# Performance work log

Measured on AMD Instinct MI355X. Metric: run time of the kernel, lower is better.

Reference implementation:

```python
import jax, jax.numpy as jnp
import numpy as np

B, S, H, NH, BLK, R = 2, 4096, 768, 12, 64, 3
D = H // NH
NB = S // BLK
PENALTY = -10000.0


def setup_inputs() -> dict:
    key = jax.random.key(0)
    ks = jax.random.split(key, 5)
    return {
        "hidden_states": jax.random.normal(ks[0], (B, S, H), dtype=jnp.float32),
        "Wq": jax.random.normal(ks[1], (H, H), dtype=jnp.float32) * 0.02,
        "Wk": jax.random.normal(ks[2], (H, H), dtype=jnp.float32) * 0.02,
        "Wv": jax.random.normal(ks[3], (H, H), dtype=jnp.float32) * 0.02,
        "band_mask": jnp.ones((B, 1, NB - 4, BLK, 3 * BLK), dtype=jnp.float32),
        "from_mask": jnp.ones((B, 1, S, 1), dtype=jnp.float32),
        "to_mask": jnp.ones((B, 1, 1, S), dtype=jnp.float32),
        "from_blocked_mask": jnp.ones((B, NB, BLK), dtype=jnp.float32),
        "to_blocked_mask": jnp.ones((B, NB, BLK), dtype=jnp.float32),
        "rand_attn": jax.random.randint(ks[4], (B, NH, NB - 2, R), 0, NB, dtype=jnp.int64),
    }


def reference(hidden_states, Wq, Wk, Wv, band_mask, from_mask, to_mask,
              from_blocked_mask, to_blocked_mask, rand_attn):
    b, s, _ = hidden_states.shape
    nb, blk, r = NB, BLK, R
    rsqrt_d = 1.0 / jnp.sqrt(jnp.float32(D))
    sm = jax.nn.softmax

    # projections -> [b, h, s, d]
    def proj(W):
        return jnp.einsum('bse,ed->bsd', hidden_states, W).reshape(b, s, NH, D).transpose(0, 2, 1, 3)
    q, k, v = proj(Wq), proj(Wk), proj(Wv)

    bq = q.reshape(b, NH, nb, blk, D)
    bk = k.reshape(b, NH, nb, blk, D)
    bv = v.reshape(b, NH, nb, blk, D)

    # gather random key/value blocks: [b, h, nb-2, r*blk, d]
    bi = jnp.arange(b)[:, None, None, None]
    hi = jnp.arange(NH)[None, :, None, None]
    gk = bk[bi, hi, rand_attn].reshape(b, NH, nb - 2, r * blk, D)
    gv = bv[bi, hi, rand_attn].reshape(b, NH, nb - 2, r * blk, D)

    # random mask: [b, h, nb-2, blk, r*blk]
    rm = to_blocked_mask[jnp.arange(b)[:, None, None, None], rand_attn]  # [b,h,nb-2,r,blk]
    rm = rm.reshape(b, NH, nb - 2, r * blk)
    rand_mask = jnp.einsum('blq,bhlk->bhlqk', from_blocked_mask[:, 1:-1], rm)

    ones_rand = jnp.ones((b, 1, 1, r * blk), dtype=to_mask.dtype)
    ones_4blk = jnp.ones((b, NH, blk, 4 * blk), dtype=rand_mask.dtype)

    # --- first (global) block: attends to everything ---
    fp = jnp.einsum('bhqd,bhkd->bhqk', bq[:, :, 0], k) * rsqrt_d + (1.0 - to_mask) * PENALTY
    fc = jnp.einsum('bhqk,bhkd->bhqd', sm(fp, axis=-1), v)[:, :, None]  # [b,h,1,blk,d]

    # --- second block: first 3 blocks + last block + random blocks ---
    sk = jnp.concatenate([bk[:, :, 0], bk[:, :, 1], bk[:, :, 2], bk[:, :, -1], gk[:, :, 0]], axis=2)
    sv = jnp.concatenate([bv[:, :, 0], bv[:, :, 1], bv[:, :, 2], bv[:, :, -1], gv[:, :, 0]], axis=2)
    sp = jnp.einsum('bhqd,bhkd->bhqk', bq[:, :, 1], sk) * rsqrt_d
    seq_pad = jnp.concatenate([to_mask[:, :, :, :3 * blk], to_mask[:, :, :, -blk:], ones_rand], axis=3)
    rand_pad = jnp.concatenate([ones_4blk, rand_mask[:, :, 0]], axis=3)
    sp = sp + (1.0 - jnp.minimum(seq_pad, rand_pad)) * PENALTY
    sc = jnp.einsum('bhqk,bhkd->bhqd', sm(sp, axis=-1), sv)[:, :, None]

    # --- middle blocks: sliding window + global first/last + random ---
    ek = jnp.concatenate([bk[:, :, 1:-3], bk[:, :, 2:-2], bk[:, :, 3:-1]], axis=3)  # [b,h,nb-4,3blk,d]
    ev = jnp.concatenate([bv[:, :, 1:-3], bv[:, :, 2:-2], bv[:, :, 3:-1]], axis=3)
    mq = bq[:, :, 2:-2]
    inner = jnp.einsum('bhlqd,bhlkd->bhlqk', mq, ek) * rsqrt_d + (1.0 - band_mask) * PENALTY
    randb = jnp.einsum('bhlqd,bhlkd->bhlqk', mq, gk[:, :, 1:-1]) * rsqrt_d + (1.0 - rand_mask[:, :, 1:-1]) * PENALTY
    firstb = jnp.einsum('bhlqd,bhkd->bhlqk', mq, bk[:, :, 0]) * rsqrt_d + (1.0 - to_mask[:, :, :, None, :blk]) * PENALTY
    lastb = jnp.einsum('bhlqd,bhkd->bhlqk', mq, bk[:, :, -1]) * rsqrt_d + (1.0 - to_mask[:, :, :, None, -blk:]) * PENALTY
    band = jnp.concatenate([firstb, inner, randb, lastb], axis=-1)  # [...,(5+r)*blk]
    aw = sm(band, axis=-1)
    ctx_mid = (jnp.einsum('bhlqk,bhlkd->bhlqd', aw[..., blk:4 * blk], ev)
               + jnp.einsum('bhlqk,bhlkd->bhlqd', aw[..., 4 * blk:-blk], gv[:, :, 1:-1])
               + jnp.einsum('bhlqk,bhkd->bhlqd', aw[..., :blk], bv[:, :, 0])
               + jnp.einsum('bhlqk,bhkd->bhlqd', aw[..., -blk:], bv[:, :, -1]))

    # --- second-last block ---
    slk = jnp.concatenate([bk[:, :, 0], bk[:, :, -3], bk[:, :, -2], bk[:, :, -1], gk[:, :, -1]], axis=2)
    slv = jnp.concatenate([bv[:, :, 0], bv[:, :, -3], bv[:, :, -2], bv[:, :, -1], gv[:, :, -1]], axis=2)
    slp = jnp.einsum('bhqd,bhkd->bhqk', bq[:, :, -2], slk) * rsqrt_d
    sl_seq_pad = jnp.concatenate([to_mask[:, :, :, :blk], to_mask[:, :, :, -3 * blk:], ones_rand], axis=3)
    sl_rand_pad = jnp.concatenate([ones_4blk, rand_mask[:, :, -1]], axis=3)
    slp = slp + (1.0 - jnp.minimum(sl_seq_pad, sl_rand_pad)) * PENALTY
    slc = jnp.einsum('bhqk,bhkd->bhqd', sm(slp, axis=-1), slv)[:, :, None]

    # --- last (global) block ---
    lp = jnp.einsum('bhqd,bhkd->bhqk', bq[:, :, -1], k) * rsqrt_d + (1.0 - to_mask) * PENALTY
    lc = jnp.einsum('bhqk,bhkd->bhqd', sm(lp, axis=-1), v)[:, :, None]

    ctx = jnp.concatenate([fc, sc, ctx_mid, slc, lc], axis=2).reshape(b, NH, s, D)
    ctx = ctx * from_mask  # [b,1,s,1] broadcast
    return ctx.transpose(0, 2, 1, 3).reshape(b, s, NH * D)
```

## Files before the change

kernel.cpp:

```cpp
#include <hip/hip_runtime.h>
#include <hip/hip_bf16.h>
#include <stdint.h>

#define NHD 12
#define SLEN 4096
#define DH 64
#define NBLK 64
#define HDIM 768
#define PEN -10000.0f
#define LOG2E 1.44269504f

typedef __bf16 bf16x8 __attribute__((ext_vector_type(8)));
typedef float f32x4 __attribute__((ext_vector_type(4)));
typedef unsigned short u16x8 __attribute__((ext_vector_type(8)));

__device__ __forceinline__ unsigned short f2bf(float x) {
    union { float f; unsigned u; } v; v.f = x;
    unsigned r = v.u + 0x7fffu + ((v.u >> 16) & 1u);
    return (unsigned short)(r >> 16);
}

__device__ __forceinline__ void gl2lds16(const void* g, void* l) {
    __builtin_amdgcn_global_load_lds(
        (const __attribute__((address_space(1))) void*)g,
        (__attribute__((address_space(3))) void*)l, 16, 0, 0);
}

__global__ void k_cast_hs(const float* __restrict__ in, unsigned short* __restrict__ out, int n8) {
    int i = blockIdx.x * blockDim.x + threadIdx.x;
    if (i >= n8) return;
    const float4* p = (const float4*)in + (size_t)i * 2;
    float4 a = p[0], b = p[1];
    u16x8 o;
    o[0]=f2bf(a.x); o[1]=f2bf(a.y); o[2]=f2bf(a.z); o[3]=f2bf(a.w);
    o[4]=f2bf(b.x); o[5]=f2bf(b.y); o[6]=f2bf(b.z); o[7]=f2bf(b.w);
    ((u16x8*)out)[i] = o;
}

__global__ void k_wt(const float* __restrict__ Wq, const float* __restrict__ Wk,
                     const float* __restrict__ Wv, unsigned short* __restrict__ wt) {
    const float* W = blockIdx.z == 0 ? Wq : (blockIdx.z == 1 ? Wk : Wv);
    unsigned short* out = wt + (size_t)blockIdx.z * HDIM * HDIM;
    __shared__ float tile[64][65];
    int t = threadIdx.x;
    int k0 = blockIdx.x * 64, n0 = blockIdx.y * 64;
    int r = t >> 2, c4 = t & 3;
#pragma unroll
    for (int j = 0; j < 16; j += 4) {
        float4 v = *(const float4*)&W[(size_t)(k0 + r) * HDIM + n0 + c4 * 16 + j];
        tile[r][c4*16+j+0] = v.x; tile[r][c4*16+j+1] = v.y;
        tile[r][c4*16+j+2] = v.z; tile[r][c4*16+j+3] = v.w;
    }
    __syncthreads();
    u16x8 o0, o1;
#pragma unroll
    for (int j = 0; j < 8; ++j) o0[j] = f2bf(tile[c4*16 + j][r]);
#pragma unroll
    for (int j = 0; j < 8; ++j) o1[j] = f2bf(tile[c4*16 + 8 + j][r]);
    *(u16x8*)&out[(size_t)(n0 + r) * HDIM + k0 + c4*16]     = o0;
    *(u16x8*)&out[(size_t)(n0 + r) * HDIM + k0 + c4*16 + 8] = o1;
}

template<bool TR>
__global__ __launch_bounds__(256) void k_proj(const unsigned short* __restrict__ hsb,
                                              const unsigned short* __restrict__ wtb,
                                              unsigned short* __restrict__ outbuf) {
    __shared__ __align__(16) unsigned short As[8192];
    __shared__ __align__(16) unsigned short Bs[8192];
    const char* Abase = (const char*)hsb;
    const char* Bbase = (const char*)(wtb + (size_t)blockIdx.z * HDIM * HDIM);
    unsigned short* out = outbuf + (size_t)blockIdx.z * (2u * NHD * SLEN * DH);
    int m0 = blockIdx.x * 128, n0 = blockIdx.y * 128;
    int t = threadIdx.x;
    int w = t >> 6, l = t & 63, g = l >> 4, c = l & 15;
    int wm = w >> 1, wn = w & 1;
    int lr = l >> 3, ls = l & 7, sw = ls ^ lr;
    int c7 = c & 7;
    f32x4 acc[4][4];
#pragma unroll
    for (int i = 0; i < 4; ++i)
#pragma unroll
        for (int j = 0; j < 4; ++j) acc[i][j] = (f32x4){0.f,0.f,0.f,0.f};

    for (int kt = 0; kt < HDIM; kt += 64) {
        __syncthreads();
#pragma unroll
        for (int i = 0; i < 4; ++i) {
            int rowb = w * 32 + i * 8;
            gl2lds16(Abase + (size_t)(m0 + rowb + lr) * 1536 + kt * 2 + sw * 16,
                     (char*)As + rowb * 128);
            gl2lds16(Bbase + (size_t)(n0 + rowb + lr) * 1536 + kt * 2 + sw * 16,
                     (char*)Bs + rowb * 128);
        }
        __syncthreads();
#pragma unroll
        for (int ks = 0; ks < 2; ++ks) {
            bf16x8 af[4], bf_[4];
#pragma unroll
            for (int mt = 0; mt < 4; ++mt)
                af[mt]  = *(const bf16x8*)((const char*)As
                            + (64*wm + 16*mt + c) * 128 + (((ks*4 + g) ^ c7) * 16));
#pragma unroll
            for (int nt = 0; nt < 4; ++nt)
                bf_[nt] = *(const bf16x8*)((const char*)Bs
                            + (64*wn + 16*nt + c) * 128 + (((ks*4 + g) ^ c7) * 16));
#pragma unroll
            for (int i = 0; i < 4; ++i)
#pragma unroll
                for (int j = 0; j < 4; ++j)
                    acc[i][j] = TR
                        ? __builtin_amdgcn_mfma_f32_16x16x32_bf16(bf_[i], af[j], acc[i][j], 0, 0, 0)
                        : __builtin_amdgcn_mfma_f32_16x16x32_bf16(af[i], bf_[j], acc[i][j], 0, 0, 0);
        }
    }
#pragma unroll
    for (int i = 0; i < 4; ++i)
#pragma unroll
        for (int j = 0; j < 4; ++j)
#pragma unroll
            for (int r2 = 0; r2 < 4; ++r2) {
                if (!TR) {
                    int m = m0 + 64*wm + 16*i + 4*g + r2;
                    int n = n0 + 64*wn + 16*j + c;
                    int bb = m >> 12, s = m & 4095;
                    int hh = n >> 6,  d = n & 63;
                    out[(((size_t)bb * NHD + hh) * SLEN + s) * DH + d] = f2bf(acc[i][j][r2]);
                } else {
                    int n = n0 + 64*wn + 16*i + 4*g + r2;
                    int m = m0 + 64*wm + 16*j + c;
                    int bb = m >> 12, s = m & 4095;
                    int hh = n >> 6,  d = n & 63;
                    out[(((size_t)bb * NHD + hh) * DH + d) * SLEN + s] = f2bf(acc[i][j][r2]);
                }
            }
}

__global__ __launch_bounds__(256) void k_attn(
    const unsigned short* __restrict__ Qb, const unsigned short* __restrict__ Kb,
    const unsigned short* __restrict__ VTb,
    const int* __restrict__ rand_attn,
    const float* __restrict__ band_mask, const float* __restrict__ from_mask,
    const float* __restrict__ to_mask, const float* __restrict__ fbm,
    const float* __restrict__ tbm,
    float* __restrict__ out, float* __restrict__ partials)
{
    __shared__ __align__(16) unsigned short Kt[2][4096];
    __shared__ __align__(16) unsigned short Vt[2][4096];
    __shared__ __align__(16) char plds[4 * 2048];

    const float SC = 0.125f * LOG2E;
    const float PL = PEN * LOG2E;
    const float THR2 = 8.0f * LOG2E;

    int i0 = blockIdx.x;
    int gid = (i0 & 7) * 234 + (i0 >> 3);
    int bh = gid / 78, task = gid - bh * 78;
    int b = bh / NHD, h = bh - b * NHD;
    int t = threadIdx.x;
    int wq = t >> 6, l = t & 63, g = l >> 4, c = l & 15;
    int lr = l >> 3, ls = l & 7, sw = ls ^ lr;

    int row, mode = 0, pslot = 0;
    int blkj[8], kvj[8], sbj[8];
#pragma unroll
    for (int j = 0; j < 8; ++j) sbj[j] = 0;
    if (task < 8) {
        row = 0; mode = 1; pslot = task;
#pragma unroll
        for (int j = 0; j < 8; ++j) { blkj[j] = task * 8 + j; kvj[j] = 0; }
    } else if (task >= 70) {
        row = 63; mode = 1; pslot = task - 70;
#pragma unroll
        for (int j = 0; j < 8; ++j) { blkj[j] = pslot * 8 + j; kvj[j] = 0; }
    } else {
        row = task - 7;
        int rbase = ((b * NHD + h) * 62 + (row - 1)) * 3;
        blkj[4] = rand_attn[rbase];
        blkj[5] = rand_attn[rbase + 1];
        blkj[6] = rand_attn[rbase + 2];
        kvj[4] = kvj[5] = kvj[6] = 2;
        blkj[0] = 0; kvj[0] = 0;
        if (row == 1) {
            blkj[1]=1;  blkj[2]=2;  blkj[3]=63; kvj[1]=kvj[2]=kvj[3]=0;
            blkj[7]=0;  kvj[7]=3;
        } else if (row == 62) {
            blkj[1]=61; blkj[2]=62; blkj[3]=63; kvj[1]=kvj[2]=kvj[3]=0;
            blkj[7]=0;  kvj[7]=3;
        } else {
            blkj[1]=row-1; blkj[2]=row; blkj[3]=row+1;
            kvj[1]=kvj[2]=kvj[3]=1; sbj[1]=0; sbj[2]=64; sbj[3]=128;
            blkj[7]=63; kvj[7]=0;
        }
    }

    size_t bhoff = (size_t)bh * SLEN * DH;
    const char* Kbase = (const char*)(Kb + bhoff);
    const char* Vbase = (const char*)(VTb + (size_t)bh * DH * SLEN);
    int q0 = row * 64 + wq * 16;

    bf16x8 qf[2];
#pragma unroll
    for (int kk = 0; kk < 2; ++kk)
        qf[kk] = *(const bf16x8*)&Qb[bhoff + (size_t)(q0 + c) * DH + kk * 32 + 8 * g];

    float fmq = fbm[(b * NBLK + row) * 64 + wq * 16 + c];
    size_t bm_base = ((size_t)(b * 60 + row - 2) * 64 + (wq * 16 + c)) * 192;
    int tm_base = b * SLEN;

    float m_run = -1e30f, l_run = 0.f;
    f32x4 o_acc[4];
#pragma unroll
    for (int dt = 0; dt < 4; ++dt) o_acc[dt] = (f32x4){0.f,0.f,0.f,0.f};

    char* myl = plds + wq * 2048 + c * 128;
    int swz = (c & 7) << 4;

    auto stage = [&](int blk, int nb) __attribute__((always_inline)) {
#pragma unroll
        for (int ii = 0; ii < 2; ++ii) {
            int i = wq * 2 + ii;
            const char* ksrc = Kbase + (size_t)blk * 8192 + (size_t)(i*8 + lr) * 128 + sw * 16;
            gl2lds16(ksrc, (char*)&Kt[nb][0] + i * 1024);
            const char* vsrc = Vbase + (size_t)(i*8 + lr) * 8192 + (size_t)blk * 128 + sw * 16;
            gl2lds16(vsrc, (char*)&Vt[nb][0] + i * 1024);
        }
    };

    auto loadpen = [&](int kv, int blk, int sb, float4* pen) __attribute__((always_inline)) {
        if (kv == 0) {
#pragma unroll
            for (int mt = 0; mt < 4; ++mt) {
                float4 mk = *(const float4*)&to_mask[tm_base + blk * 64 + mt * 16 + 4 * g];
                pen[mt].x = (1.f - mk.x) * PL; pen[mt].y = (1.f - mk.y) * PL;
                pen[mt].z = (1.f - mk.z) * PL; pen[mt].w = (1.f - mk.w) * PL;
            }
        } else if (kv == 1) {
#pragma unroll
            for (int mt = 0; mt < 4; ++mt) {
                float4 mk = *(const float4*)&band_mask[bm_base + sb + mt * 16 + 4 * g];
                pen[mt].x = (1.f - mk.x) * PL; pen[mt].y = (1.f - mk.y) * PL;
                pen[mt].z = (1.f - mk.z) * PL; pen[mt].w = (1.f - mk.w) * PL;
            }
        } else if (kv == 2) {
#pragma unroll
            for (int mt = 0; mt < 4; ++mt) {
                float4 tb = *(const float4*)&tbm[(size_t)(b * NBLK + blk) * 64 + mt * 16 + 4 * g];
                pen[mt].x = (1.f - fmq * tb.x) * PL; pen[mt].y = (1.f - fmq * tb.y) * PL;
                pen[mt].z = (1.f - fmq * tb.z) * PL; pen[mt].w = (1.f - fmq * tb.w) * PL;
            }
        }
    };

    auto compute = [&](int kv, int nb, const float4* pen) __attribute__((always_inline)) {
        if (kv == 3) return;
        int c7 = c & 7;
        bf16x8 kf[4][2];
#pragma unroll
        for (int mt = 0; mt < 4; ++mt)
#pragma unroll
            for (int kk = 0; kk < 2; ++kk)
                kf[mt][kk] = *(const bf16x8*)((const char*)&Kt[nb][0]
                              + (mt*16 + c) * 128 + (((kk*4 + g) ^ c7) * 16));

        f32x4 sa[4];
#pragma unroll
        for (int mt = 0; mt < 4; ++mt) sa[mt] = (f32x4){0.f,0.f,0.f,0.f};
#pragma unroll
        for (int kk = 0; kk < 2; ++kk)
#pragma unroll
            for (int mt = 0; mt < 4; ++mt)
                sa[mt] = __builtin_amdgcn_mfma_f32_16x16x32_bf16(kf[mt][kk], qf[kk], sa[mt], 0, 0, 0);

#pragma unroll
        for (int mt = 0; mt < 4; ++mt) {
            sa[mt][0] = sa[mt][0] * SC + pen[mt].x;
            sa[mt][1] = sa[mt][1] * SC + pen[mt].y;
            sa[mt][2] = sa[mt][2] * SC + pen[mt].z;
            sa[mt][3] = sa[mt][3] * SC + pen[mt].w;
        }

        float pm = -1e30f;
#pragma unroll
        for (int mt = 0; mt < 4; ++mt)
#pragma unroll
            for (int r2 = 0; r2 < 4; ++r2) pm = fmaxf(pm, sa[mt][r2]);
        pm = fmaxf(pm, __shfl_xor(pm, 16));
        pm = fmaxf(pm, __shfl_xor(pm, 32));
        if (__ballot(pm > m_run + THR2)) {
            bool need = pm > m_run + THR2;
            float mnew = need ? pm : m_run;
            float scale = exp2f(m_run - mnew);
            m_run = mnew;
            l_run *= scale;
#pragma unroll
            for (int dt = 0; dt < 4; ++dt)
#pragma unroll
                for (int r2 = 0; r2 < 4; ++r2) o_acc[dt][r2] *= scale;
        }

        float rs = 0.f;
#pragma unroll
        for (int mt = 0; mt < 4; ++mt)
#pragma unroll
            for (int r2 = 0; r2 < 4; ++r2) {
                float e = exp2f(sa[mt][r2] - m_run);
                sa[mt][r2] = e;
                rs += e;
            }
        rs += __shfl_xor(rs, 16);
        rs += __shfl_xor(rs, 32);
        l_run += rs;

#pragma unroll
        for (int mt = 0; mt < 4; ++mt) {
            union { __bf16 hh[4]; unsigned long long u; } pk_;
            pk_.hh[0] = (__bf16)sa[mt][0]; pk_.hh[1] = (__bf16)sa[mt][1];
            pk_.hh[2] = (__bf16)sa[mt][2]; pk_.hh[3] = (__bf16)sa[mt][3];
            *(unsigned long long*)(myl + ((mt * 32 + g * 8) ^ swz)) = pk_.u;
        }
        asm volatile("" ::: "memory");
        bf16x8 pf0 = *(const bf16x8*)(myl + ((g * 16) ^ swz));
        bf16x8 pf1 = *(const bf16x8*)(myl + ((64 + g * 16) ^ swz));

#pragma unroll
        for (int dt = 0; dt < 4; ++dt) {
            bf16x8 v0 = *(const bf16x8*)((const char*)&Vt[nb][0]
                          + (dt*16 + c) * 128 + ((g ^ c7) * 16));
            bf16x8 v1 = *(const bf16x8*)((const char*)&Vt[nb][0]
                          + (dt*16 + c) * 128 + (((4 + g) ^ c7) * 16));
            o_acc[dt] = __builtin_amdgcn_mfma_f32_16x16x32_bf16(v0, pf0, o_acc[dt], 0, 0, 0);
            o_acc[dt] = __builtin_amdgcn_mfma_f32_16x16x32_bf16(v1, pf1, o_acc[dt], 0, 0, 0);
        }
    };

    float4 penA[4], penB[4];
    stage(blkj[0], 0);
    loadpen(kvj[0], blkj[0], sbj[0], penA);
    __syncthreads();
#pragma unroll
    for (int tt = 0; tt < 8; ++tt) {
        if (tt < 7) {
            stage(blkj[tt + 1], (tt & 1) ^ 1);
            loadpen(kvj[tt + 1], blkj[tt + 1], sbj[tt + 1], (tt & 1) ? penA : penB);
        }
        compute(kvj[tt], tt & 1, (tt & 1) ? penB : penA);
        __syncthreads();
    }

    if (mode == 0) {
        int s = q0 + c;
        float fm = from_mask[b * SLEN + s];
        float inv = fm / l_run;
        size_t obase = ((size_t)b * SLEN + s) * HDIM + h * DH;
#pragma unroll
        for (int dt = 0; dt < 4; ++dt) {
            float4 val;
            val.x = o_acc[dt][0] * inv;
            val.y = o_acc[dt][1] * inv;
            val.z = o_acc[dt][2] * inv;
            val.w = o_acc[dt][3] * inv;
            *(float4*)&out[obase + dt * 16 + 4 * g] = val;
        }
    } else {
        float* pb = partials + (size_t)((bh * 2 + (row == 63 ? 1 : 0)) * 8 + pslot) * 4224;
        int q = wq * 16 + c;
#pragma unroll
        for (int dt = 0; dt < 4; ++dt) {
            float4 val;
            val.x = o_acc[dt][0]; val.y = o_acc[dt][1];
            val.z = o_acc[dt][2]; val.w = o_acc[dt][3];
            *(float4*)&pb[q * 64 + dt * 16 + 4 * g] = val;
        }
        if (g == 0) {
            pb[4096 + q] = m_run;
            pb[4160 + q] = l_run;
        }
    }
}

__global__ void k_combine(const float* __restrict__ partials, const float* __restrict__ from_mask,
                          float* __restrict__ out) {
    int gid = blockIdx.x;
    int bh = gid >> 1, rb = gid & 1;
    int b = bh / NHD, h = bh - b * NHD;
    int t = threadIdx.x;
    int q = t >> 2, dc = (t & 3) * 16;
    const float* base = partials + (size_t)gid * 8 * 4224;
    float M = -1e30f;
#pragma unroll
    for (int i = 0; i < 8; ++i) M = fmaxf(M, base[i*4224 + 4096 + q]);
    float L = 0.f, cx[16];
#pragma unroll
    for (int j = 0; j < 16; ++j) cx[j] = 0.f;
    for (int i = 0; i < 8; ++i) {
        float w = exp2f(base[i*4224 + 4096 + q] - M);
        L += base[i*4224 + 4160 + q] * w;
#pragma unroll
        for (int j = 0; j < 16; ++j) cx[j] += base[i*4224 + q*64 + dc + j] * w;
    }
    int s = (rb ? 4032 : 0) + q;
    float fm = from_mask[b * SLEN + s];
    float inv = fm / L;
#pragma unroll
    for (int j = 0; j < 16; ++j)
        out[((size_t)b * SLEN + s) * HDIM + h * DH + dc + j] = cx[j] * inv;
}

extern "C" void kernel_launch(void* const* d_in, const int* in_sizes, int n_in,
                              void* d_out, int out_size, void* d_ws, size_t ws_size,
                              hipStream_t stream) {
    const float* hs    = (const float*)d_in[0];
    const float* Wq    = (const float*)d_in[1];
    const float* Wk    = (const float*)d_in[2];
    const float* Wv    = (const float*)d_in[3];
    const float* band  = (const float*)d_in[4];
    const float* fromm = (const float*)d_in[5];
    const float* tom   = (const float*)d_in[6];
    const float* fbm   = (const float*)d_in[7];
    const float* tbm   = (const float*)d_in[8];
    const int*   ra    = (const int*)d_in[9];
    float* out = (float*)d_out;

    char* ws = (char*)d_ws;
    unsigned short* hsb = (unsigned short*)(ws);
    unsigned short* wtb = (unsigned short*)(ws + 12582912);
    unsigned short* qkv = (unsigned short*)(ws + 16121856);
    float* partials     = (float*)(ws + 53870592);

    k_cast_hs<<<3072, 256, 0, stream>>>(hs, hsb, 786432);
    k_wt<<<dim3(12, 12, 3), 256, 0, stream>>>(Wq, Wk, Wv, wtb);
    k_proj<false><<<dim3(64, 6, 2), 256, 0, stream>>>(hsb, wtb, qkv);
    k_proj<true><<<dim3(64, 6, 1), 256, 0, stream>>>(hsb, wtb + 2 * HDIM * HDIM,
                                                     qkv + 2 * 6291456);
    k_attn<<<1872, 256, 0, stream>>>(qkv, qkv + 6291456, qkv + 2 * 6291456, ra,
                                     band, fromm, tom, fbm, tbm, out, partials);
    k_combine<<<48, 256, 0, stream>>>(partials, fromm, out);
}
```

Measured before the change: 109.7 us.

## Merge QKV projection launches and single-buffer V tile in attention kernel

The Q/K and transposed-V projection kernels are folded into one launch, with the weight selected from blockIdx.y and the transposed branch chosen at runtime. In the attention kernel, V is now single-buffered in LDS and is staged only after the PV step of the previous block, with an extra barrier per iteration. This cuts LDS use so more workgroups may fit per CU and removes one launch. In exchange it serializes the V load with compute and adds synchronization, and the projection kernel now carries a runtime branch around its MFMA loop.

After: 138.8 us. +26.6%, slower.

```diff
diff --git a/kernel.cpp b/kernel.cpp
--- a/kernel.cpp
+++ b/kernel.cpp
@@ -61,16 +61,16 @@
     *(u16x8*)&out[(size_t)(n0 + r) * HDIM + k0 + c4*16 + 8] = o1;
 }
 
-template<bool TR>
 __global__ __launch_bounds__(256) void k_proj(const unsigned short* __restrict__ hsb,
                                               const unsigned short* __restrict__ wtb,
-                                              unsigned short* __restrict__ outbuf) {
+                                              unsigned short* __restrict__ qkv) {
     __shared__ __align__(16) unsigned short As[8192];
     __shared__ __align__(16) unsigned short Bs[8192];
+    int z = blockIdx.y / 6, ny = blockIdx.y - z * 6;
     const char* Abase = (const char*)hsb;
-    const char* Bbase = (const char*)(wtb + (size_t)blockIdx.z * HDIM * HDIM);
-    unsigned short* out = outbuf + (size_t)blockIdx.z * (2u * NHD * SLEN * DH);
-    int m0 = blockIdx.x * 128, n0 = blockIdx.y * 128;
+    const char* Bbase = (const char*)(wtb + (size_t)z * HDIM * HDIM);
+    unsigned short* out = qkv + (size_t)z * (2u * NHD * SLEN * DH);
+    int m0 = blockIdx.x * 128, n0 = ny * 128;
     int t = threadIdx.x;
     int w = t >> 6, l = t & 63, g = l >> 4, c = l & 15;
     int wm = w >> 1, wn = w & 1;
@@ -104,13 +104,19 @@
             for (int nt = 0; nt < 4; ++nt)
                 bf_[nt] = *(const bf16x8*)((const char*)Bs
                             + (64*wn + 16*nt + c) * 128 + (((ks*4 + g) ^ c7) * 16));
-#pragma unroll
-            for (int i = 0; i < 4; ++i)
-#pragma unroll
-                for (int j = 0; j < 4; ++j)
-                    acc[i][j] = TR
-                        ? __builtin_amdgcn_mfma_f32_16x16x32_bf16(bf_[i], af[j], acc[i][j], 0, 0, 0)
-                        : __builtin_amdgcn_mfma_f32_16x16x32_bf16(af[i], bf_[j], acc[i][j], 0, 0, 0);
+            if (z != 2) {
+#pragma unroll
+                for (int i = 0; i < 4; ++i)
+#pragma unroll
+                    for (int j = 0; j < 4; ++j)
+                        acc[i][j] = __builtin_amdgcn_mfma_f32_16x16x32_bf16(af[i], bf_[j], acc[i][j], 0, 0, 0);
+            } else {
+#pragma unroll
+                for (int i = 0; i < 4; ++i)
+#pragma unroll
+                    for (int j = 0; j < 4; ++j)
+                        acc[i][j] = __builtin_amdgcn_mfma_f32_16x16x32_bf16(bf_[i], af[j], acc[i][j], 0, 0, 0);
+            }
         }
     }
 #pragma unroll
@@ -119,7 +125,7 @@
         for (int j = 0; j < 4; ++j)
 #pragma unroll
             for (int r2 = 0; r2 < 4; ++r2) {
-                if (!TR) {
+                if (z != 2) {
                     int m = m0 + 64*wm + 16*i + 4*g + r2;
                     int n = n0 + 64*wn + 16*j + c;
                     int bb = m >> 12, s = m & 4095;
@@ -145,7 +151,7 @@
     float* __restrict__ out, float* __restrict__ partials)
 {
     __shared__ __align__(16) unsigned short Kt[2][4096];
-    __shared__ __align__(16) unsigned short Vt[2][4096];
+    __shared__ __align__(16) unsigned short Vt[4096];
     __shared__ __align__(16) char plds[4 * 2048];
 
     const float SC = 0.125f * LOG2E;
@@ -215,14 +221,20 @@
     char* myl = plds + wq * 2048 + c * 128;
     int swz = (c & 7) << 4;
 
-    auto stage = [&](int blk, int nb) __attribute__((always_inline)) {
+    auto stageK = [&](int blk, int nb) __attribute__((always_inline)) {
 #pragma unroll
         for (int ii = 0; ii < 2; ++ii) {
             int i = wq * 2 + ii;
-            const char* ksrc = Kbase + (size_t)blk * 8192 + (size_t)(i*8 + lr) * 128 + sw * 16;
-            gl2lds16(ksrc, (char*)&Kt[nb][0] + i * 1024);
-            const char* vsrc = Vbase + (size_t)(i*8 + lr) * 8192 + (size_t)blk * 128 + sw * 16;
-            gl2lds16(vsrc, (char*)&Vt[nb][0] + i * 1024);
+            gl2lds16(Kbase + (size_t)blk * 8192 + (size_t)(i*8 + lr) * 128 + sw * 16,
+                     (char*)&Kt[nb][0] + i * 1024);
+        }
+    };
+    auto stageV = [&](int blk) __attribute__((always_inline)) {
+#pragma unroll
+        for (int ii = 0; ii < 2; ++ii) {
+            int i = wq * 2 + ii;
+            gl2lds16(Vbase + (size_t)(i*8 + lr) * 8192 + (size_t)blk * 128 + sw * 16,
+                     (char*)Vt + i * 1024);
         }
     };
 
@@ -251,8 +263,7 @@
         }
     };
 
-    auto compute = [&](int kv, int nb, const float4* pen) __attribute__((always_inline)) {
-        if (kv == 3) return;
+    auto qk_sm = [&](int nb, const float4* pen) __attribute__((always_inline)) {
         int c7 = c & 7;
         bf16x8 kf[4][2];
 #pragma unroll
@@ -261,7 +272,6 @@
             for (int kk = 0; kk < 2; ++kk)
                 kf[mt][kk] = *(const bf16x8*)((const char*)&Kt[nb][0]
                               + (mt*16 + c) * 128 + (((kk*4 + g) ^ c7) * 16));
-
         f32x4 sa[4];
 #pragma unroll
         for (int mt = 0; mt < 4; ++mt) sa[mt] = (f32x4){0.f,0.f,0.f,0.f};
@@ -270,7 +280,6 @@
 #pragma unroll
             for (int mt = 0; mt < 4; ++mt)
                 sa[mt] = __builtin_amdgcn_mfma_f32_16x16x32_bf16(kf[mt][kk], qf[kk], sa[mt], 0, 0, 0);
-
 #pragma unroll
         for (int mt = 0; mt < 4; ++mt) {
             sa[mt][0] = sa[mt][0] * SC + pen[mt].x;
@@ -278,7 +287,6 @@
             sa[mt][2] = sa[mt][2] * SC + pen[mt].z;
             sa[mt][3] = sa[mt][3] * SC + pen[mt].w;
         }
-
         float pm = -1e30f;
 #pragma unroll
         for (int mt = 0; mt < 4; ++mt)
@@ -297,7 +305,6 @@
 #pragma unroll
                 for (int r2 = 0; r2 < 4; ++r2) o_acc[dt][r2] *= scale;
         }
-
         float rs = 0.f;
 #pragma unroll
         for (int mt = 0; mt < 4; ++mt)
@@ -310,7 +317,6 @@
         rs += __shfl_xor(rs, 16);
         rs += __shfl_xor(rs, 32);
         l_run += rs;
-
 #pragma unroll
         for (int mt = 0; mt < 4; ++mt) {
             union { __bf16 hh[4]; unsigned long long u; } pk_;
@@ -319,14 +325,17 @@
             *(unsigned long long*)(myl + ((mt * 32 + g * 8) ^ swz)) = pk_.u;
         }
         asm volatile("" ::: "memory");
+    };
+
+    auto pv = [&]() __attribute__((always_inline)) {
+        int c7 = c & 7;
         bf16x8 pf0 = *(const bf16x8*)(myl + ((g * 16) ^ swz));
         bf16x8 pf1 = *(const bf16x8*)(myl + ((64 + g * 16) ^ swz));
-
 #pragma unroll
         for (int dt = 0; dt < 4; ++dt) {
-            bf16x8 v0 = *(const bf16x8*)((const char*)&Vt[nb][0]
+            bf16x8 v0 = *(const bf16x8*)((const char*)Vt
                           + (dt*16 + c) * 128 + ((g ^ c7) * 16));
-            bf16x8 v1 = *(const bf16x8*)((const char*)&Vt[nb][0]
+            bf16x8 v1 = *(const bf16x8*)((const char*)Vt
                           + (dt*16 + c) * 128 + (((4 + g) ^ c7) * 16));
             o_acc[dt] = __builtin_amdgcn_mfma_f32_16x16x32_bf16(v0, pf0, o_acc[dt], 0, 0, 0);
             o_acc[dt] = __builtin_amdgcn_mfma_f32_16x16x32_bf16(v1, pf1, o_acc[dt], 0, 0, 0);
@@ -334,17 +343,23 @@
     };
 
     float4 penA[4], penB[4];
-    stage(blkj[0], 0);
+    stageK(blkj[0], 0);
+    stageV(blkj[0]);
     loadpen(kvj[0], blkj[0], sbj[0], penA);
     __syncthreads();
 #pragma unroll
     for (int tt = 0; tt < 8; ++tt) {
+        int nb = tt & 1;
         if (tt < 7) {
-            stage(blkj[tt + 1], (tt & 1) ^ 1);
-            loadpen(kvj[tt + 1], blkj[tt + 1], sbj[tt + 1], (tt & 1) ? penA : penB);
-        }
-        compute(kvj[tt], tt & 1, (tt & 1) ? penB : penA);
+            stageK(blkj[tt + 1], nb ^ 1);
+            loadpen(kvj[tt + 1], blkj[tt + 1], sbj[tt + 1], nb ? penA : penB);
+        }
+        bool active = (kvj[tt] != 3);
+        if (active) qk_sm(nb, nb ? penB : penA);
         __syncthreads();
+        if (active) pv();
+        __syncthreads();
+        if (tt < 7) stageV(blkj[tt + 1]);
     }
 
     if (mode == 0) {
@@ -429,9 +444,7 @@
 
     k_cast_hs<<<3072, 256, 0, stream>>>(hs, hsb, 786432);
     k_wt<<<dim3(12, 12, 3), 256, 0, stream>>>(Wq, Wk, Wv, wtb);
-    k_proj<false><<<dim3(64, 6, 2), 256, 0, stream>>>(hsb, wtb, qkv);
-    k_proj<true><<<dim3(64, 6, 1), 256, 0, stream>>>(hsb, wtb + 2 * HDIM * HDIM,
-                                                     qkv + 2 * 6291456);
+    k_proj<<<dim3(64, 18), 256, 0, stream>>>(hsb, wtb, qkv);
     k_attn<<<1872, 256, 0, stream>>>(qkv, qkv + 6291456, qkv + 2 * 6291456, ra,
                                      band, fromm, tom, fbm, tbm, out, partials);
     k_combine<<<48, 256, 0, stream>>>(partials, fromm, out);
```

## Process two key blocks per attention step with 128-wide KV tiles

Applied to the files above, without the earlier changes.

The attention loop now stages two 64-key blocks at a time into doubled LDS buffers and runs one softmax/PV update over 128 keys. This halves the loop iterations, barriers and online-softmax rescale checks. V is staged in a new interleaved, swizzled layout so the PV MFMAs can use K=128. In exchange LDS use doubles, which may lower occupancy, and the penalty loads are no longer prefetched one step ahead of compute. When the second block is inactive, its probability slots are zero-filled, so some MFMA work is wasted.

Result: slower. 120.2 us (+9.6%).

```diff
diff --git a/kernel.cpp b/kernel.cpp
--- a/kernel.cpp
+++ b/kernel.cpp
@@ -144,9 +144,9 @@
     const float* __restrict__ tbm,
     float* __restrict__ out, float* __restrict__ partials)
 {
-    __shared__ __align__(16) unsigned short Kt[2][4096];
-    __shared__ __align__(16) unsigned short Vt[2][4096];
-    __shared__ __align__(16) char plds[4 * 2048];
+    __shared__ __align__(16) unsigned short Kt[2][8192];
+    __shared__ __align__(16) unsigned short Vt[2][8192];
+    __shared__ __align__(16) char plds[4 * 4096];
 
     const float SC = 0.125f * LOG2E;
     const float PL = PEN * LOG2E;
@@ -159,6 +159,7 @@
     int t = threadIdx.x;
     int wq = t >> 6, l = t & 63, g = l >> 4, c = l & 15;
     int lr = l >> 3, ls = l & 7, sw = ls ^ lr;
+    int c7 = c & 7;
 
     int row, mode = 0, pslot = 0;
     int blkj[8], kvj[8], sbj[8];
@@ -212,17 +213,26 @@
 #pragma unroll
     for (int dt = 0; dt < 4; ++dt) o_acc[dt] = (f32x4){0.f,0.f,0.f,0.f};
 
-    char* myl = plds + wq * 2048 + c * 128;
-    int swz = (c & 7) << 4;
-
-    auto stage = [&](int blk, int nb) __attribute__((always_inline)) {
-#pragma unroll
-        for (int ii = 0; ii < 2; ++ii) {
-            int i = wq * 2 + ii;
-            const char* ksrc = Kbase + (size_t)blk * 8192 + (size_t)(i*8 + lr) * 128 + sw * 16;
-            gl2lds16(ksrc, (char*)&Kt[nb][0] + i * 1024);
-            const char* vsrc = Vbase + (size_t)(i*8 + lr) * 8192 + (size_t)blk * 128 + sw * 16;
-            gl2lds16(vsrc, (char*)&Vt[nb][0] + i * 1024);
+    char* myl = plds + wq * 4096 + c * 256;
+    int swz = c7 << 4;
+
+    auto stage = [&](int blkA, int blkB, int nb) __attribute__((always_inline)) {
+#pragma unroll
+        for (int ii = 0; ii < 4; ++ii) {
+            int ch = wq * 4 + ii;
+            {
+                int blk = (ch >> 3) ? blkB : blkA;
+                int keyrow = (ch & 7) * 8 + lr;
+                gl2lds16(Kbase + (size_t)blk * 8192 + (size_t)keyrow * 128 + sw * 16,
+                         (char*)&Kt[nb][0] + ch * 1024);
+            }
+            {
+                int drow = ch * 4 + (l >> 4);
+                int sl = (l & 15) ^ ((4 * (ch & 1) + (l >> 4)) & 7);
+                int blk = (sl & 8) ? blkB : blkA;
+                gl2lds16(Vbase + (size_t)drow * 8192 + (size_t)blk * 128 + (sl & 7) * 16,
+                         (char*)&Vt[nb][0] + ch * 1024);
+            }
         }
     };
 
@@ -251,39 +261,53 @@
         }
     };
 
-    auto compute = [&](int kv, int nb, const float4* pen) __attribute__((always_inline)) {
-        if (kv == 3) return;
-        int c7 = c & 7;
-        bf16x8 kf[4][2];
+    auto step128 = [&](int nb, bool actB, const float4* pen0, const float4* pen1)
+        __attribute__((always_inline)) {
+        const char* Kl = (const char*)&Kt[nb][0];
+        f32x4 sa0[4], sa1[4];
+#pragma unroll
+        for (int mt = 0; mt < 4; ++mt) {
+            bf16x8 k0 = *(const bf16x8*)(Kl + (16*mt + c) * 128 + ((g ^ c7) * 16));
+            bf16x8 k1 = *(const bf16x8*)(Kl + (16*mt + c) * 128 + (((4 + g) ^ c7) * 16));
+            f32x4 s = __builtin_amdgcn_mfma_f32_16x16x32_bf16(k0, qf[0], (f32x4){0,0,0,0}, 0, 0, 0);
+            sa0[mt] = __builtin_amdgcn_mfma_f32_16x16x32_bf16(k1, qf[1], s, 0, 0, 0);
+        }
+        if (actB) {
+#pragma unroll
+            for (int mt = 0; mt < 4; ++mt) {
+                bf16x8 k0 = *(const bf16x8*)(Kl + (64 + 16*mt + c) * 128 + ((g ^ c7) * 16));
+                bf16x8 k1 = *(const bf16x8*)(Kl + (64 + 16*mt + c) * 128 + (((4 + g) ^ c7) * 16));
+                f32x4 s = __builtin_amdgcn_mfma_f32_16x16x32_bf16(k0, qf[0], (f32x4){0,0,0,0}, 0, 0, 0);
+                sa1[mt] = __builtin_amdgcn_mfma_f32_16x16x32_bf16(k1, qf[1], s, 0, 0, 0);
+            }
+        }
+#pragma unroll
+        for (int mt = 0; mt < 4; ++mt) {
+            sa0[mt][0] = sa0[mt][0] * SC + pen0[mt].x;
+            sa0[mt][1] = sa0[mt][1] * SC + pen0[mt].y;
+            sa0[mt][2] = sa0[mt][2] * SC + pen0[mt].z;
+            sa0[mt][3] = sa0[mt][3] * SC + pen0[mt].w;
+        }
+        if (actB) {
+#pragma unroll
+            for (int mt = 0; mt < 4; ++mt) {
+                sa1[mt][0] = sa1[mt][0] * SC + pen1[mt].x;
+                sa1[mt][1] = sa1[mt][1] * SC + pen1[mt].y;
+                sa1[mt][2] = sa1[mt][2] * SC + pen1[mt].z;
+                sa1[mt][3] = sa1[mt][3] * SC + pen1[mt].w;
+            }
+        }
+        float pm = -1e30f;
 #pragma unroll
         for (int mt = 0; mt < 4; ++mt)
 #pragma unroll
-            for (int kk = 0; kk < 2; ++kk)
-                kf[mt][kk] = *(const bf16x8*)((const char*)&Kt[nb][0]
-                              + (mt*16 + c) * 128 + (((kk*4 + g) ^ c7) * 16));
-
-        f32x4 sa[4];
-#pragma unroll
-        for (int mt = 0; mt < 4; ++mt) sa[mt] = (f32x4){0.f,0.f,0.f,0.f};
-#pragma unroll
-        for (int kk = 0; kk < 2; ++kk)
+            for (int r2 = 0; r2 < 4; ++r2) pm = fmaxf(pm, sa0[mt][r2]);
+        if (actB) {
 #pragma unroll
             for (int mt = 0; mt < 4; ++mt)
-                sa[mt] = __builtin_amdgcn_mfma_f32_16x16x32_bf16(kf[mt][kk], qf[kk], sa[mt], 0, 0, 0);
-
-#pragma unroll
-        for (int mt = 0; mt < 4; ++mt) {
-            sa[mt][0] = sa[mt][0] * SC + pen[mt].x;
-            sa[mt][1] = sa[mt][1] * SC + pen[mt].y;
-            sa[mt][2] = sa[mt][2] * SC + pen[mt].z;
-            sa[mt][3] = sa[mt][3] * SC + pen[mt].w;
-        }
-
-        float pm = -1e30f;
-#pragma unroll
-        for (int mt = 0; mt < 4; ++mt)
-#pragma unroll
-            for (int r2 = 0; r2 < 4; ++r2) pm = fmaxf(pm, sa[mt][r2]);
+#pragma unroll
+                for (int r2 = 0; r2 < 4; ++r2) pm = fmaxf(pm, sa1[mt][r2]);
+        }
         pm = fmaxf(pm, __shfl_xor(pm, 16));
         pm = fmaxf(pm, __shfl_xor(pm, 32));
         if (__ballot(pm > m_run + THR2)) {
@@ -297,53 +321,73 @@
 #pragma unroll
                 for (int r2 = 0; r2 < 4; ++r2) o_acc[dt][r2] *= scale;
         }
-
         float rs = 0.f;
 #pragma unroll
         for (int mt = 0; mt < 4; ++mt)
 #pragma unroll
             for (int r2 = 0; r2 < 4; ++r2) {
-                float e = exp2f(sa[mt][r2] - m_run);
-                sa[mt][r2] = e;
-                rs += e;
-            }
+                float e = exp2f(sa0[mt][r2] - m_run);
+                sa0[mt][r2] = e; rs += e;
+            }
+        if (actB) {
+#pragma unroll
+            for (int mt = 0; mt < 4; ++mt)
+#pragma unroll
+                for (int r2 = 0; r2 < 4; ++r2) {
+                    float e = exp2f(sa1[mt][r2] - m_run);
+                    sa1[mt][r2] = e; rs += e;
+                }
+        }
         rs += __shfl_xor(rs, 16);
         rs += __shfl_xor(rs, 32);
         l_run += rs;
-
 #pragma unroll
         for (int mt = 0; mt < 4; ++mt) {
             union { __bf16 hh[4]; unsigned long long u; } pk_;
-            pk_.hh[0] = (__bf16)sa[mt][0]; pk_.hh[1] = (__bf16)sa[mt][1];
-            pk_.hh[2] = (__bf16)sa[mt][2]; pk_.hh[3] = (__bf16)sa[mt][3];
+            pk_.hh[0] = (__bf16)sa0[mt][0]; pk_.hh[1] = (__bf16)sa0[mt][1];
+            pk_.hh[2] = (__bf16)sa0[mt][2]; pk_.hh[3] = (__bf16)sa0[mt][3];
             *(unsigned long long*)(myl + ((mt * 32 + g * 8) ^ swz)) = pk_.u;
         }
+        if (actB) {
+#pragma unroll
+            for (int mt = 0; mt < 4; ++mt) {
+                union { __bf16 hh[4]; unsigned long long u; } pk_;
+                pk_.hh[0] = (__bf16)sa1[mt][0]; pk_.hh[1] = (__bf16)sa1[mt][1];
+                pk_.hh[2] = (__bf16)sa1[mt][2]; pk_.hh[3] = (__bf16)sa1[mt][3];
+                *(unsigned long long*)(myl + ((128 + mt * 32 + g * 8) ^ swz)) = pk_.u;
+            }
+        } else {
+#pragma unroll
+            for (int mt = 0; mt < 4; ++mt)
+                *(unsigned long long*)(myl + ((128 + mt * 32 + g * 8) ^ swz)) = 0ULL;
+        }
         asm volatile("" ::: "memory");
-        bf16x8 pf0 = *(const bf16x8*)(myl + ((g * 16) ^ swz));
-        bf16x8 pf1 = *(const bf16x8*)(myl + ((64 + g * 16) ^ swz));
-
+        bf16x8 pa[4];
+#pragma unroll
+        for (int kk = 0; kk < 4; ++kk)
+            pa[kk] = *(const bf16x8*)(myl + ((kk * 64 + g * 16) ^ swz));
+        const char* Vl = (const char*)&Vt[nb][0];
 #pragma unroll
         for (int dt = 0; dt < 4; ++dt) {
-            bf16x8 v0 = *(const bf16x8*)((const char*)&Vt[nb][0]
-                          + (dt*16 + c) * 128 + ((g ^ c7) * 16));
-            bf16x8 v1 = *(const bf16x8*)((const char*)&Vt[nb][0]
-                          + (dt*16 + c) * 128 + (((4 + g) ^ c7) * 16));
-            o_acc[dt] = __builtin_amdgcn_mfma_f32_16x16x32_bf16(v0, pf0, o_acc[dt], 0, 0, 0);
-            o_acc[dt] = __builtin_amdgcn_mfma_f32_16x16x32_bf16(v1, pf1, o_acc[dt], 0, 0, 0);
+#pragma unroll
+            for (int kk = 0; kk < 4; ++kk) {
+                bf16x8 v = *(const bf16x8*)(Vl + (dt*16 + c) * 256 + ((kk*64 + 16*g) ^ swz));
+                o_acc[dt] = __builtin_amdgcn_mfma_f32_16x16x32_bf16(v, pa[kk], o_acc[dt], 0, 0, 0);
+            }
         }
     };
 
-    float4 penA[4], penB[4];
-    stage(blkj[0], 0);
-    loadpen(kvj[0], blkj[0], sbj[0], penA);
+    float4 pen0[4], pen1[4];
+    stage(blkj[0], blkj[1], 0);
     __syncthreads();
 #pragma unroll
-    for (int tt = 0; tt < 8; ++tt) {
-        if (tt < 7) {
-            stage(blkj[tt + 1], (tt & 1) ^ 1);
-            loadpen(kvj[tt + 1], blkj[tt + 1], sbj[tt + 1], (tt & 1) ? penA : penB);
-        }
-        compute(kvj[tt], tt & 1, (tt & 1) ? penB : penA);
+    for (int tt = 0; tt < 4; ++tt) {
+        int nb = tt & 1;
+        if (tt < 3) stage(blkj[2*tt + 2], blkj[2*tt + 3], nb ^ 1);
+        bool actB = (kvj[2*tt + 1] != 3);
+        loadpen(kvj[2*tt], blkj[2*tt], sbj[2*tt], pen0);
+        if (actB) loadpen(kvj[2*tt + 1], blkj[2*tt + 1], sbj[2*tt + 1], pen1);
+        step128(nb, actB, pen0, pen1);
         __syncthreads();
     }
 
```
